# Kernel optimization log

Hardware: AMD Instinct MI355X
Metric: run time of the kernel (lower is better)

Reference implementation:

```python
import jax, jax.numpy as jnp
import numpy as np

BETA = 0.5

def setup_inputs() -> dict:
    key = jax.random.key(0)
    ks = jax.random.split(key, 10)
    B, H = 4096, 200
    ITEM, REGION = 100000, 1000
    D, HID = 128, 64  # embed_size, hidden_size
    half = D // 2
    history = jax.random.randint(ks[0], (B, H), 0, ITEM)
    target = jax.random.randint(ks[1], (B,), 0, ITEM)
    history_region = jax.random.randint(ks[2], (B, H), 0, REGION)
    target_region = jax.random.randint(ks[3], (B,), 0, REGION)
    W_hist = jax.random.normal(ks[4], (ITEM, half), jnp.float32) * 0.01
    W_tgt = jax.random.normal(ks[5], (ITEM, half), jnp.float32) * 0.01
    W_reg = jax.random.normal(ks[6], (REGION, half), jnp.float32) * 0.01
    W1 = jax.random.normal(ks[7], (D, HID), jnp.float32) * (1.0 / np.sqrt(D))
    b1 = jnp.zeros((HID,), jnp.float32)
    W2 = jax.random.normal(ks[8], (HID,), jnp.float32) * (1.0 / np.sqrt(HID))
    return {"history": history, "target": target,
            "history_region": history_region, "target_region": target_region,
            "W_hist": W_hist, "W_tgt": W_tgt, "W_reg": W_reg,
            "W1": W1, "b1": b1, "W2": W2}

def reference(history, target, history_region, target_region,
              W_hist, W_tgt, W_reg, W1, b1, W2):
    # gather + concat: [B,H,D] and [B,D]
    h = jnp.concatenate([W_hist[history], W_reg[history_region]], axis=-1)
    t = jnp.concatenate([W_tgt[target], W_reg[target_region]], axis=-1)
    inp = h * t[:, None, :]                      # [B,H,D]
    r1 = jax.nn.relu(inp @ W1 + b1)              # [B,H,HID] (dropout = identity at eval)
    logits = r1 @ W2                             # [B,H]
    mask = (history != target[:, None]).astype(logits.dtype)
    exp_A = jnp.exp(logits) * mask               # [B,H]
    exp_sum = jnp.sum(exp_A, axis=-1) ** BETA    # [B], beta-power normalization
    attn = exp_A / exp_sum[:, None]              # [B,H]
    pred = jnp.einsum('bhd,bd->b', h * attn[..., None], t)
    return jax.nn.sigmoid(pred)
```

## Files before the change

### kernel.cpp

```cpp
#include <hip/hip_runtime.h>
#include <math.h>

#define NB        4096
#define NH        200
#define HIST_ROWS 100000
#define REG_ROWS  1000
#define NTILES    13

typedef __attribute__((ext_vector_type(8))) short short8;
typedef __attribute__((ext_vector_type(4))) float f32x4;

__device__ __forceinline__ unsigned short f2bf(float x) {
    union { float f; unsigned u; } v; v.f = x;
    unsigned r = v.u + 0x7FFF + ((v.u >> 16) & 1);
    return (unsigned short)(r >> 16);
}

__global__ __launch_bounds__(256) void prep_tables(
    const float* __restrict__ Wh, const float* __restrict__ Wr,
    const float* __restrict__ W1,
    unsigned short* __restrict__ tab, float* __restrict__ W1F)
{
    const int total4 = (HIST_ROWS + REG_ROWS) * 16;
    const int HE4    = HIST_ROWS * 16;
    for (int i = blockIdx.x * blockDim.x + threadIdx.x; i < total4;
         i += gridDim.x * blockDim.x) {
        const float4 v = (i < HE4) ? ((const float4*)Wh)[i]
                                   : ((const float4*)Wr)[i - HE4];
        ushort4 o;
        o.x = f2bf(v.x); o.y = f2bf(v.y); o.z = f2bf(v.z); o.w = f2bf(v.w);
        ((ushort4*)tab)[i] = o;
    }
    if (blockIdx.x == 0) {
        for (int i = threadIdx.x; i < 1024; i += 256) {
            const int frag = i >> 6, c = i & 63;
            const int nt = frag >> 2, ks = frag & 3, q = c >> 4, l = c & 15;
            const int k0 = ks * 32 + q * 8, n = nt * 16 + l;
            float tmp[8];
            #pragma unroll
            for (int j = 0; j < 8; ++j) tmp[j] = W1[(k0 + j) * 64 + n];
            float4* dst = (float4*)(W1F + i * 8);
            dst[0] = make_float4(tmp[0], tmp[1], tmp[2], tmp[3]);
            dst[1] = make_float4(tmp[4], tmp[5], tmp[6], tmp[7]);
        }
    }
}

__device__ __forceinline__ void epi_store(
    const f32x4* accT, const float* w2v, const float* b1v,
    int tl, int quad, int l15, float* logit_lds, float* s_lds)
{
    float part[4] = {0.f, 0.f, 0.f, 0.f};
    #pragma unroll
    for (int nt = 0; nt < 4; ++nt)
        #pragma unroll
        for (int r = 0; r < 4; ++r)
            part[r] += fmaxf(accT[nt][r] + b1v[nt], 0.f) * w2v[nt];
    #pragma unroll
    for (int r = 0; r < 4; ++r) {
        part[r] += __shfl_xor(part[r], 1);
        part[r] += __shfl_xor(part[r], 2);
        part[r] += __shfl_xor(part[r], 4);
        part[r] += __shfl_xor(part[r], 8);
    }
    if (l15 == 0) {
        const int jg = tl * 16 + quad * 4;
        #pragma unroll
        for (int r = 0; r < 4; ++r) {
            logit_lds[jg + r] = part[r];
            s_lds[jg + r]     = accT[4][r];
        }
    }
}

template <bool BT>
__global__ __launch_bounds__(256, 3) void nais_mfma5(
    const int*   __restrict__ history,
    const int*   __restrict__ target,
    const int*   __restrict__ history_region,
    const int*   __restrict__ target_region,
    const float* __restrict__ W_hist,
    const float* __restrict__ W_tgt,
    const float* __restrict__ W_reg,
    const float* __restrict__ W1,
    const float* __restrict__ b1,
    const float* __restrict__ W2,
    const unsigned short* __restrict__ tab,
    const float* __restrict__ W1F,
    float*       __restrict__ out)
{
    __shared__ int hist_lds[224];
    __shared__ int hreg_lds[224];
    __shared__ __align__(16) float t_lds[128];
    __shared__ __align__(16) unsigned short Bf[20 * 512];
    __shared__ float logit_lds[208];
    __shared__ float s_lds[208];
    __shared__ float red_e[4], red_p[4];

    const int b   = blockIdx.x;
    const int tid = threadIdx.x;
    const int tgt = target[b];

    if (tid < 224) {
        const int jj = tid < NH ? tid : NH - 1;
        hist_lds[tid] = history[b * NH + jj];
        hreg_lds[tid] = history_region[b * NH + jj];
    }
    if (tid < 64) {
        t_lds[tid] = W_tgt[(size_t)tgt * 64 + tid];
    } else if (tid < 128) {
        t_lds[tid] = W_reg[(size_t)target_region[b] * 64 + (tid - 64)];
    }
    __syncthreads();

    const int lane = tid & 63, wv = tid >> 6;
    const int l15  = lane & 15, quad = lane >> 4;

    const int  tl0 = wv, tl1 = wv + 4, tl2 = wv + 8, tl3 = wv + 12;
    const bool has3 = (tl3 < NTILES);
    const int  j0 = tl0 * 16 + l15;
    const int  j1 = tl1 * 16 + l15;
    const int  j2 = tl2 * 16 + l15;
    const int  j3 = has3 ? (tl3 * 16 + l15) : j2;

    const unsigned short* tabr = tab + (size_t)HIST_ROWS * 64;
    const unsigned short *p0h, *p0r, *p1h, *p1r, *p2h, *p2r, *p3h, *p3r;
    short8 A0[4], A1[4];
    if (BT) {
        p0h = tab  + (size_t)hist_lds[j0] * 64 + quad * 8;
        p0r = tabr + (size_t)hreg_lds[j0] * 64 + quad * 8;
        p1h = tab  + (size_t)hist_lds[j1] * 64 + quad * 8;
        p1r = tabr + (size_t)hreg_lds[j1] * 64 + quad * 8;
        p2h = tab  + (size_t)hist_lds[j2] * 64 + quad * 8;
        p2r = tabr + (size_t)hreg_lds[j2] * 64 + quad * 8;
        p3h = tab  + (size_t)hist_lds[j3] * 64 + quad * 8;
        p3r = tabr + (size_t)hreg_lds[j3] * 64 + quad * 8;
        #pragma unroll
        for (int ks = 0; ks < 4; ++ks) {
            A0[ks] = *reinterpret_cast<const short8*>((ks < 2 ? p0h : p0r) + (ks & 1) * 32);
            A1[ks] = *reinterpret_cast<const short8*>((ks < 2 ? p1h : p1r) + (ks & 1) * 32);
        }
    }

    #pragma unroll
    for (int v = 0; v < 4; ++v) {
        const int i  = tid + v * 256;
        const int ks = (i >> 6) & 3, q = (i >> 4) & 3;
        const int k0 = ks * 32 + q * 8;
        const float4 t0 = *(const float4*)(t_lds + k0);
        const float4 t1 = *(const float4*)(t_lds + k0 + 4);
        float4 w0, w1;
        if (BT) {
            w0 = ((const float4*)W1F)[i * 2];
            w1 = ((const float4*)W1F)[i * 2 + 1];
        } else {
            const int nt = i >> 8, l = i & 15, n = nt * 16 + l;
            float tmp[8];
            #pragma unroll
            for (int j = 0; j < 8; ++j) tmp[j] = W1[(k0 + j) * 64 + n];
            w0 = make_float4(tmp[0], tmp[1], tmp[2], tmp[3]);
            w1 = make_float4(tmp[4], tmp[5], tmp[6], tmp[7]);
        }
        short8 o;
        o[0] = (short)f2bf(w0.x * t0.x); o[1] = (short)f2bf(w0.y * t0.y);
        o[2] = (short)f2bf(w0.z * t0.z); o[3] = (short)f2bf(w0.w * t0.w);
        o[4] = (short)f2bf(w1.x * t1.x); o[5] = (short)f2bf(w1.y * t1.y);
        o[6] = (short)f2bf(w1.z * t1.z); o[7] = (short)f2bf(w1.w * t1.w);
        *reinterpret_cast<short8*>(&Bf[i * 8]) = o;
    }
    {
        const int i  = 1024 + tid;
        const int ks = tid >> 6, c = tid & 63, q = c >> 4, l = c & 15;
        const int k0 = ks * 32 + q * 8;
        short8 o;
        #pragma unroll
        for (int j = 0; j < 8; ++j)
            o[j] = (l == 0) ? (short)f2bf(t_lds[k0 + j]) : (short)0;
        *reinterpret_cast<short8*>(&Bf[i * 8]) = o;
    }
    __syncthreads();

    float w2v[4], b1v[4];
    #pragma unroll
    for (int nt = 0; nt < 4; ++nt) {
        w2v[nt] = W2[nt * 16 + l15];
        b1v[nt] = b1[nt * 16 + l15];
    }

    f32x4 acc[2][5];
    #pragma unroll
    for (int tt = 0; tt < 2; ++tt)
        #pragma unroll
        for (int nt = 0; nt < 5; ++nt) acc[tt][nt] = (f32x4){0.f, 0.f, 0.f, 0.f};

    #pragma unroll
    for (int ks = 0; ks < 4; ++ks) {
        short8 bf[5];
        #pragma unroll
        for (int nt = 0; nt < 5; ++nt)
            bf[nt] = *reinterpret_cast<const short8*>(
                &Bf[((nt * 4 + ks) * 64 + quad * 16 + l15) * 8]);
        if (!BT) {
            const float* q0 = ((ks < 2) ? (W_hist + (size_t)hist_lds[j0] * 64)
                                        : (W_reg  + (size_t)hreg_lds[j0] * 64)) + quad * 8 + (ks & 1) * 32;
            const float* q1 = ((ks < 2) ? (W_hist + (size_t)hist_lds[j1] * 64)
                                        : (W_reg  + (size_t)hreg_lds[j1] * 64)) + quad * 8 + (ks & 1) * 32;
            const float4 v0 = *(const float4*)q0, v1 = *(const float4*)(q0 + 4);
            const float4 u0 = *(const float4*)q1, u1 = *(const float4*)(q1 + 4);
            A0[ks][0]=(short)f2bf(v0.x); A0[ks][1]=(short)f2bf(v0.y); A0[ks][2]=(short)f2bf(v0.z); A0[ks][3]=(short)f2bf(v0.w);
            A0[ks][4]=(short)f2bf(v1.x); A0[ks][5]=(short)f2bf(v1.y); A0[ks][6]=(short)f2bf(v1.z); A0[ks][7]=(short)f2bf(v1.w);
            A1[ks][0]=(short)f2bf(u0.x); A1[ks][1]=(short)f2bf(u0.y); A1[ks][2]=(short)f2bf(u0.z); A1[ks][3]=(short)f2bf(u0.w);
            A1[ks][4]=(short)f2bf(u1.x); A1[ks][5]=(short)f2bf(u1.y); A1[ks][6]=(short)f2bf(u1.z); A1[ks][7]=(short)f2bf(u1.w);
        }
        #pragma unroll
        for (int nt = 0; nt < 5; ++nt)
            acc[0][nt] = __builtin_amdgcn_mfma_f32_16x16x32_bf16(A0[ks], bf[nt], acc[0][nt], 0, 0, 0);
        #pragma unroll
        for (int nt = 0; nt < 5; ++nt)
            acc[1][nt] = __builtin_amdgcn_mfma_f32_16x16x32_bf16(A1[ks], bf[nt], acc[1][nt], 0, 0, 0);
    }

    short8 A2[4], A3[4];
    if (BT) {
        #pragma unroll
        for (int ks = 0; ks < 4; ++ks) {
            A2[ks] = *reinterpret_cast<const short8*>((ks < 2 ? p2h : p2r) + (ks & 1) * 32);
            A3[ks] = *reinterpret_cast<const short8*>((ks < 2 ? p3h : p3r) + (ks & 1) * 32);
        }
    }

    epi_store(acc[0], w2v, b1v, tl0, quad, l15, logit_lds, s_lds);
    epi_store(acc[1], w2v, b1v, tl1, quad, l15, logit_lds, s_lds);

    #pragma unroll
    for (int tt = 0; tt < 2; ++tt)
        #pragma unroll
        for (int nt = 0; nt < 5; ++nt) acc[tt][nt] = (f32x4){0.f, 0.f, 0.f, 0.f};

    #pragma unroll
    for (int ks = 0; ks < 4; ++ks) {
        short8 bf[5];
        #pragma unroll
        for (int nt = 0; nt < 5; ++nt)
            bf[nt] = *reinterpret_cast<const short8*>(
                &Bf[((nt * 4 + ks) * 64 + quad * 16 + l15) * 8]);
        if (!BT) {
            const float* q0 = ((ks < 2) ? (W_hist + (size_t)hist_lds[j2] * 64)
                                        : (W_reg  + (size_t)hreg_lds[j2] * 64)) + quad * 8 + (ks & 1) * 32;
            const float* q1 = ((ks < 2) ? (W_hist + (size_t)hist_lds[j3] * 64)
                                        : (W_reg  + (size_t)hreg_lds[j3] * 64)) + quad * 8 + (ks & 1) * 32;
            const float4 v0 = *(const float4*)q0, v1 = *(const float4*)(q0 + 4);
            const float4 u0 = *(const float4*)q1, u1 = *(const float4*)(q1 + 4);
            A2[ks][0]=(short)f2bf(v0.x); A2[ks][1]=(short)f2bf(v0.y); A2[ks][2]=(short)f2bf(v0.z); A2[ks][3]=(short)f2bf(v0.w);
            A2[ks][4]=(short)f2bf(v1.x); A2[ks][5]=(short)f2bf(v1.y); A2[ks][6]=(short)f2bf(v1.z); A2[ks][7]=(short)f2bf(v1.w);
            A3[ks][0]=(short)f2bf(u0.x); A3[ks][1]=(short)f2bf(u0.y); A3[ks][2]=(short)f2bf(u0.z); A3[ks][3]=(short)f2bf(u0.w);
            A3[ks][4]=(short)f2bf(u1.x); A3[ks][5]=(short)f2bf(u1.y); A3[ks][6]=(short)f2bf(u1.z); A3[ks][7]=(short)f2bf(u1.w);
        }
        #pragma unroll
        for (int nt = 0; nt < 5; ++nt)
            acc[0][nt] = __builtin_amdgcn_mfma_f32_16x16x32_bf16(A2[ks], bf[nt], acc[0][nt], 0, 0, 0);
        if (has3) {
            #pragma unroll
            for (int nt = 0; nt < 5; ++nt)
                acc[1][nt] = __builtin_amdgcn_mfma_f32_16x16x32_bf16(A3[ks], bf[nt], acc[1][nt], 0, 0, 0);
        }
    }

    epi_store(acc[0], w2v, b1v, tl2, quad, l15, logit_lds, s_lds);
    if (has3) epi_store(acc[1], w2v, b1v, tl3, quad, l15, logit_lds, s_lds);
    __syncthreads();

    float e = 0.f, p = 0.f;
    if (tid < NH) {
        const float ex = (hist_lds[tid] != tgt) ? expf(logit_lds[tid]) : 0.f;
        e = ex;
        p = ex * s_lds[tid];
    }
    #pragma unroll
    for (int off = 32; off > 0; off >>= 1) {
        e += __shfl_down(e, off);
        p += __shfl_down(p, off);
    }
    if (lane == 0) { red_e[wv] = e; red_p[wv] = p; }
    __syncthreads();
    if (tid == 0) {
        const float E = red_e[0] + red_e[1] + red_e[2] + red_e[3];
        const float P = red_p[0] + red_p[1] + red_p[2] + red_p[3];
        const float pred = P / sqrtf(E);
        out[b] = 1.f / (1.f + expf(-pred));
    }
}

extern "C" void kernel_launch(void* const* d_in, const int* in_sizes, int n_in,
                              void* d_out, int out_size, void* d_ws, size_t ws_size,
                              hipStream_t stream) {
    const int*   history        = (const int*)  d_in[0];
    const int*   target         = (const int*)  d_in[1];
    const int*   history_region = (const int*)  d_in[2];
    const int*   target_region  = (const int*)  d_in[3];
    const float* W_hist         = (const float*)d_in[4];
    const float* W_tgt          = (const float*)d_in[5];
    const float* W_reg          = (const float*)d_in[6];
    const float* W1             = (const float*)d_in[7];
    const float* b1             = (const float*)d_in[8];
    const float* W2             = (const float*)d_in[9];
    float* out = (float*)d_out;

    const size_t tab_bytes = (size_t)(HIST_ROWS + REG_ROWS) * 64 * 2;
    const size_t need = tab_bytes + 1024 * 8 * 4;
    if (ws_size >= need) {
        unsigned short* tab = (unsigned short*)d_ws;
        float* W1F = (float*)((char*)d_ws + tab_bytes);
        prep_tables<<<2048, 256, 0, stream>>>(W_hist, W_reg, W1, tab, W1F);
        nais_mfma5<true><<<NB, 256, 0, stream>>>(history, target, history_region, target_region,
                                                 W_hist, W_tgt, W_reg, W1, b1, W2, tab, W1F, out);
    } else {
        nais_mfma5<false><<<NB, 256, 0, stream>>>(history, target, history_region, target_region,
                                                  W_hist, W_tgt, W_reg, W1, b1, W2, nullptr, nullptr, out);
    }
}
```

Baseline: 145.7 us.

## Drop bf16 table prep kernel; gather fp32 rows directly with prefetch and packed cvt

Removes the separate prep kernel that converted the full embedding tables to bf16 every call. The main kernel now gathers fp32 rows directly, converting them with a packed bf16 conversion builtin where available. Rows for the second tile pair are issued before the first pair's epilogue to hide latency. This trades the full-table conversion pass for double the gather bytes per row and higher register pressure from the fp32 prefetch buffers.

```diff
diff --git a/kernel.cpp b/kernel.cpp
--- a/kernel.cpp
+++ b/kernel.cpp
@@ -3,8 +3,6 @@
 
 #define NB        4096
 #define NH        200
-#define HIST_ROWS 100000
-#define REG_ROWS  1000
 #define NTILES    13
 
 typedef __attribute__((ext_vector_type(8))) short short8;
@@ -16,34 +14,24 @@
     return (unsigned short)(r >> 16);
 }
 
-__global__ __launch_bounds__(256) void prep_tables(
-    const float* __restrict__ Wh, const float* __restrict__ Wr,
-    const float* __restrict__ W1,
-    unsigned short* __restrict__ tab, float* __restrict__ W1F)
-{
-    const int total4 = (HIST_ROWS + REG_ROWS) * 16;
-    const int HE4    = HIST_ROWS * 16;
-    for (int i = blockIdx.x * blockDim.x + threadIdx.x; i < total4;
-         i += gridDim.x * blockDim.x) {
-        const float4 v = (i < HE4) ? ((const float4*)Wh)[i]
-                                   : ((const float4*)Wr)[i - HE4];
-        ushort4 o;
-        o.x = f2bf(v.x); o.y = f2bf(v.y); o.z = f2bf(v.z); o.w = f2bf(v.w);
-        ((ushort4*)tab)[i] = o;
-    }
-    if (blockIdx.x == 0) {
-        for (int i = threadIdx.x; i < 1024; i += 256) {
-            const int frag = i >> 6, c = i & 63;
-            const int nt = frag >> 2, ks = frag & 3, q = c >> 4, l = c & 15;
-            const int k0 = ks * 32 + q * 8, n = nt * 16 + l;
-            float tmp[8];
-            #pragma unroll
-            for (int j = 0; j < 8; ++j) tmp[j] = W1[(k0 + j) * 64 + n];
-            float4* dst = (float4*)(W1F + i * 8);
-            dst[0] = make_float4(tmp[0], tmp[1], tmp[2], tmp[3]);
-            dst[1] = make_float4(tmp[4], tmp[5], tmp[6], tmp[7]);
-        }
-    }
+#if __has_builtin(__builtin_amdgcn_cvt_pk_bf16_f32)
+typedef __attribute__((ext_vector_type(2))) __bf16 bf16x2;
+__device__ __forceinline__ unsigned pack2bf(float a, float b) {
+    union { bf16x2 v; unsigned u; } c;
+    c.v = __builtin_amdgcn_cvt_pk_bf16_f32(a, b);
+    return c.u;
+}
+#else
+__device__ __forceinline__ unsigned pack2bf(float a, float b) {
+    return (unsigned)f2bf(a) | ((unsigned)f2bf(b) << 16);
+}
+#endif
+
+__device__ __forceinline__ short8 pack_frag(const float4 v0, const float4 v1) {
+    union { short8 s; unsigned u[4]; } o;
+    o.u[0] = pack2bf(v0.x, v0.y); o.u[1] = pack2bf(v0.z, v0.w);
+    o.u[2] = pack2bf(v1.x, v1.y); o.u[3] = pack2bf(v1.z, v1.w);
+    return o.s;
 }
 
 __device__ __forceinline__ void epi_store(
@@ -73,8 +61,19 @@
     }
 }
 
-template <bool BT>
-__global__ __launch_bounds__(256, 3) void nais_mfma5(
+__device__ __forceinline__ void issue_row(
+    const float* __restrict__ W_hist, const float* __restrict__ W_reg,
+    const int* hist_lds, const int* hreg_lds, int j, int quad, float4* F)
+{
+    const float* ph = W_hist + (size_t)hist_lds[j] * 64 + quad * 8;
+    const float* pr = W_reg  + (size_t)hreg_lds[j] * 64 + quad * 8;
+    F[0] = *(const float4*)(ph);      F[1] = *(const float4*)(ph + 4);
+    F[2] = *(const float4*)(ph + 32); F[3] = *(const float4*)(ph + 36);
+    F[4] = *(const float4*)(pr);      F[5] = *(const float4*)(pr + 4);
+    F[6] = *(const float4*)(pr + 32); F[7] = *(const float4*)(pr + 36);
+}
+
+__global__ __launch_bounds__(256, 3) void nais_fused8(
     const int*   __restrict__ history,
     const int*   __restrict__ target,
     const int*   __restrict__ history_region,
@@ -85,8 +84,6 @@
     const float* __restrict__ W1,
     const float* __restrict__ b1,
     const float* __restrict__ W2,
-    const unsigned short* __restrict__ tab,
-    const float* __restrict__ W1F,
     float*       __restrict__ out)
 {
     __shared__ int hist_lds[224];
@@ -123,60 +120,39 @@
     const int  j2 = tl2 * 16 + l15;
     const int  j3 = has3 ? (tl3 * 16 + l15) : j2;
 
-    const unsigned short* tabr = tab + (size_t)HIST_ROWS * 64;
-    const unsigned short *p0h, *p0r, *p1h, *p1r, *p2h, *p2r, *p3h, *p3r;
-    short8 A0[4], A1[4];
-    if (BT) {
-        p0h = tab  + (size_t)hist_lds[j0] * 64 + quad * 8;
-        p0r = tabr + (size_t)hreg_lds[j0] * 64 + quad * 8;
-        p1h = tab  + (size_t)hist_lds[j1] * 64 + quad * 8;
-        p1r = tabr + (size_t)hreg_lds[j1] * 64 + quad * 8;
-        p2h = tab  + (size_t)hist_lds[j2] * 64 + quad * 8;
-        p2r = tabr + (size_t)hreg_lds[j2] * 64 + quad * 8;
-        p3h = tab  + (size_t)hist_lds[j3] * 64 + quad * 8;
-        p3r = tabr + (size_t)hreg_lds[j3] * 64 + quad * 8;
-        #pragma unroll
-        for (int ks = 0; ks < 4; ++ks) {
-            A0[ks] = *reinterpret_cast<const short8*>((ks < 2 ? p0h : p0r) + (ks & 1) * 32);
-            A1[ks] = *reinterpret_cast<const short8*>((ks < 2 ? p1h : p1r) + (ks & 1) * 32);
-        }
-    }
+    float4 F0[8], F1[8];
+    issue_row(W_hist, W_reg, hist_lds, hreg_lds, j0, quad, F0);
+    issue_row(W_hist, W_reg, hist_lds, hreg_lds, j1, quad, F1);
 
     #pragma unroll
     for (int v = 0; v < 4; ++v) {
         const int i  = tid + v * 256;
-        const int ks = (i >> 6) & 3, q = (i >> 4) & 3;
-        const int k0 = ks * 32 + q * 8;
+        const int nt = i >> 8, ks = (i >> 6) & 3, q = (i >> 4) & 3, l = i & 15;
+        const int k0 = ks * 32 + q * 8, n = nt * 16 + l;
         const float4 t0 = *(const float4*)(t_lds + k0);
         const float4 t1 = *(const float4*)(t_lds + k0 + 4);
-        float4 w0, w1;
-        if (BT) {
-            w0 = ((const float4*)W1F)[i * 2];
-            w1 = ((const float4*)W1F)[i * 2 + 1];
-        } else {
-            const int nt = i >> 8, l = i & 15, n = nt * 16 + l;
-            float tmp[8];
-            #pragma unroll
-            for (int j = 0; j < 8; ++j) tmp[j] = W1[(k0 + j) * 64 + n];
-            w0 = make_float4(tmp[0], tmp[1], tmp[2], tmp[3]);
-            w1 = make_float4(tmp[4], tmp[5], tmp[6], tmp[7]);
-        }
-        short8 o;
-        o[0] = (short)f2bf(w0.x * t0.x); o[1] = (short)f2bf(w0.y * t0.y);
-        o[2] = (short)f2bf(w0.z * t0.z); o[3] = (short)f2bf(w0.w * t0.w);
-        o[4] = (short)f2bf(w1.x * t1.x); o[5] = (short)f2bf(w1.y * t1.y);
-        o[6] = (short)f2bf(w1.z * t1.z); o[7] = (short)f2bf(w1.w * t1.w);
-        *reinterpret_cast<short8*>(&Bf[i * 8]) = o;
+        float w[8];
+        #pragma unroll
+        for (int j = 0; j < 8; ++j) w[j] = W1[(k0 + j) * 64 + n];
+        union { short8 s; unsigned u[4]; } ob;
+        ob.u[0] = pack2bf(w[0] * t0.x, w[1] * t0.y);
+        ob.u[1] = pack2bf(w[2] * t0.z, w[3] * t0.w);
+        ob.u[2] = pack2bf(w[4] * t1.x, w[5] * t1.y);
+        ob.u[3] = pack2bf(w[6] * t1.z, w[7] * t1.w);
+        *reinterpret_cast<short8*>(&Bf[i * 8]) = ob.s;
     }
     {
         const int i  = 1024 + tid;
         const int ks = tid >> 6, c = tid & 63, q = c >> 4, l = c & 15;
         const int k0 = ks * 32 + q * 8;
-        short8 o;
-        #pragma unroll
-        for (int j = 0; j < 8; ++j)
-            o[j] = (l == 0) ? (short)f2bf(t_lds[k0 + j]) : (short)0;
-        *reinterpret_cast<short8*>(&Bf[i * 8]) = o;
+        const float4 t0 = *(const float4*)(t_lds + k0);
+        const float4 t1 = *(const float4*)(t_lds + k0 + 4);
+        union { short8 s; unsigned u[4]; } ob;
+        ob.u[0] = (l == 0) ? pack2bf(t0.x, t0.y) : 0u;
+        ob.u[1] = (l == 0) ? pack2bf(t0.z, t0.w) : 0u;
+        ob.u[2] = (l == 0) ? pack2bf(t1.x, t1.y) : 0u;
+        ob.u[3] = (l == 0) ? pack2bf(t1.z, t1.w) : 0u;
+        *reinterpret_cast<short8*>(&Bf[i * 8]) = ob.s;
     }
     __syncthreads();
 
@@ -200,34 +176,19 @@
         for (int nt = 0; nt < 5; ++nt)
             bf[nt] = *reinterpret_cast<const short8*>(
                 &Bf[((nt * 4 + ks) * 64 + quad * 16 + l15) * 8]);
-        if (!BT) {
-            const float* q0 = ((ks < 2) ? (W_hist + (size_t)hist_lds[j0] * 64)
-                                        : (W_reg  + (size_t)hreg_lds[j0] * 64)) + quad * 8 + (ks & 1) * 32;
-            const float* q1 = ((ks < 2) ? (W_hist + (size_t)hist_lds[j1] * 64)
-                                        : (W_reg  + (size_t)hreg_lds[j1] * 64)) + quad * 8 + (ks & 1) * 32;
-            const float4 v0 = *(const float4*)q0, v1 = *(const float4*)(q0 + 4);
-            const float4 u0 = *(const float4*)q1, u1 = *(const float4*)(q1 + 4);
-            A0[ks][0]=(short)f2bf(v0.x); A0[ks][1]=(short)f2bf(v0.y); A0[ks][2]=(short)f2bf(v0.z); A0[ks][3]=(short)f2bf(v0.w);
-            A0[ks][4]=(short)f2bf(v1.x); A0[ks][5]=(short)f2bf(v1.y); A0[ks][6]=(short)f2bf(v1.z); A0[ks][7]=(short)f2bf(v1.w);
-            A1[ks][0]=(short)f2bf(u0.x); A1[ks][1]=(short)f2bf(u0.y); A1[ks][2]=(short)f2bf(u0.z); A1[ks][3]=(short)f2bf(u0.w);
-            A1[ks][4]=(short)f2bf(u1.x); A1[ks][5]=(short)f2bf(u1.y); A1[ks][6]=(short)f2bf(u1.z); A1[ks][7]=(short)f2bf(u1.w);
-        }
-        #pragma unroll
-        for (int nt = 0; nt < 5; ++nt)
-            acc[0][nt] = __builtin_amdgcn_mfma_f32_16x16x32_bf16(A0[ks], bf[nt], acc[0][nt], 0, 0, 0);
-        #pragma unroll
-        for (int nt = 0; nt < 5; ++nt)
-            acc[1][nt] = __builtin_amdgcn_mfma_f32_16x16x32_bf16(A1[ks], bf[nt], acc[1][nt], 0, 0, 0);
-    }
-
-    short8 A2[4], A3[4];
-    if (BT) {
-        #pragma unroll
-        for (int ks = 0; ks < 4; ++ks) {
-            A2[ks] = *reinterpret_cast<const short8*>((ks < 2 ? p2h : p2r) + (ks & 1) * 32);
-            A3[ks] = *reinterpret_cast<const short8*>((ks < 2 ? p3h : p3r) + (ks & 1) * 32);
-        }
-    }
+        const short8 a0 = pack_frag(F0[2 * ks], F0[2 * ks + 1]);
+        const short8 a1 = pack_frag(F1[2 * ks], F1[2 * ks + 1]);
+        #pragma unroll
+        for (int nt = 0; nt < 5; ++nt)
+            acc[0][nt] = __builtin_amdgcn_mfma_f32_16x16x32_bf16(a0, bf[nt], acc[0][nt], 0, 0, 0);
+        #pragma unroll
+        for (int nt = 0; nt < 5; ++nt)
+            acc[1][nt] = __builtin_amdgcn_mfma_f32_16x16x32_bf16(a1, bf[nt], acc[1][nt], 0, 0, 0);
+    }
+
+    float4 F2[8], F3[8];
+    issue_row(W_hist, W_reg, hist_lds, hreg_lds, j2, quad, F2);
+    issue_row(W_hist, W_reg, hist_lds, hreg_lds, j3, quad, F3);
 
     epi_store(acc[0], w2v, b1v, tl0, quad, l15, logit_lds, s_lds);
     epi_store(acc[1], w2v, b1v, tl1, quad, l15, logit_lds, s_lds);
@@ -244,25 +205,15 @@
         for (int nt = 0; nt < 5; ++nt)
             bf[nt] = *reinterpret_cast<const short8*>(
                 &Bf[((nt * 4 + ks) * 64 + quad * 16 + l15) * 8]);
-        if (!BT) {
-            const float* q0 = ((ks < 2) ? (W_hist + (size_t)hist_lds[j2] * 64)
-                                        : (W_reg  + (size_t)hreg_lds[j2] * 64)) + quad * 8 + (ks & 1) * 32;
-            const float* q1 = ((ks < 2) ? (W_hist + (size_t)hist_lds[j3] * 64)
-                                        : (W_reg  + (size_t)hreg_lds[j3] * 64)) + quad * 8 + (ks & 1) * 32;
-            const float4 v0 = *(const float4*)q0, v1 = *(const float4*)(q0 + 4);
-            const float4 u0 = *(const float4*)q1, u1 = *(const float4*)(q1 + 4);
-            A2[ks][0]=(short)f2bf(v0.x); A2[ks][1]=(short)f2bf(v0.y); A2[ks][2]=(short)f2bf(v0.z); A2[ks][3]=(short)f2bf(v0.w);
-            A2[ks][4]=(short)f2bf(v1.x); A2[ks][5]=(short)f2bf(v1.y); A2[ks][6]=(short)f2bf(v1.z); A2[ks][7]=(short)f2bf(v1.w);
-            A3[ks][0]=(short)f2bf(u0.x); A3[ks][1]=(short)f2bf(u0.y); A3[ks][2]=(short)f2bf(u0.z); A3[ks][3]=(short)f2bf(u0.w);
-            A3[ks][4]=(short)f2bf(u1.x); A3[ks][5]=(short)f2bf(u1.y); A3[ks][6]=(short)f2bf(u1.z); A3[ks][7]=(short)f2bf(u1.w);
-        }
-        #pragma unroll
-        for (int nt = 0; nt < 5; ++nt)
-            acc[0][nt] = __builtin_amdgcn_mfma_f32_16x16x32_bf16(A2[ks], bf[nt], acc[0][nt], 0, 0, 0);
+        const short8 a0 = pack_frag(F2[2 * ks], F2[2 * ks + 1]);
+        const short8 a1 = pack_frag(F3[2 * ks], F3[2 * ks + 1]);
+        #pragma unroll
+        for (int nt = 0; nt < 5; ++nt)
+            acc[0][nt] = __builtin_amdgcn_mfma_f32_16x16x32_bf16(a0, bf[nt], acc[0][nt], 0, 0, 0);
         if (has3) {
             #pragma unroll
             for (int nt = 0; nt < 5; ++nt)
-                acc[1][nt] = __builtin_amdgcn_mfma_f32_16x16x32_bf16(A3[ks], bf[nt], acc[1][nt], 0, 0, 0);
+                acc[1][nt] = __builtin_amdgcn_mfma_f32_16x16x32_bf16(a1, bf[nt], acc[1][nt], 0, 0, 0);
         }
     }
 
@@ -306,16 +257,6 @@
     const float* W2             = (const float*)d_in[9];
     float* out = (float*)d_out;
 
-    const size_t tab_bytes = (size_t)(HIST_ROWS + REG_ROWS) * 64 * 2;
-    const size_t need = tab_bytes + 1024 * 8 * 4;
-    if (ws_size >= need) {
-        unsigned short* tab = (unsigned short*)d_ws;
-        float* W1F = (float*)((char*)d_ws + tab_bytes);
-        prep_tables<<<2048, 256, 0, stream>>>(W_hist, W_reg, W1, tab, W1F);
-        nais_mfma5<true><<<NB, 256, 0, stream>>>(history, target, history_region, target_region,
-                                                 W_hist, W_tgt, W_reg, W1, b1, W2, tab, W1F, out);
-    } else {
-        nais_mfma5<false><<<NB, 256, 0, stream>>>(history, target, history_region, target_region,
-                                                  W_hist, W_tgt, W_reg, W1, b1, W2, nullptr, nullptr, out);
-    }
-}
+    nais_fused8<<<NB, 256, 0, stream>>>(history, target, history_region, target_region,
+                                        W_hist, W_tgt, W_reg, W1, b1, W2, out);
+}
```

After: 170.9 us. 1.17x slower.
